# Performance work log

Measured on AMD Instinct MI355X. Metric: run time of the kernel, lower is better.

## Reference

```python
import jax, jax.numpy as jnp
import numpy as np

ALPHA = 0.5
EPS = 1e-6


def setup_inputs() -> dict:
    key = jax.random.key(0)
    k1, k2, k3 = jax.random.split(key, 3)
    B, N = 8192, 4096
    y_pred = jax.random.uniform(k1, (B, N), dtype=jnp.float32)
    y_true = jax.random.randint(k2, (B, N), 0, 2).astype(jnp.float32)
    depth_weights = jax.random.uniform(k3, (B, N), dtype=jnp.float32)
    return {"y_pred": y_pred, "y_true": y_true, "depth_weights": depth_weights}


def reference(y_pred, y_true, depth_weights):
    B, N = y_true.shape
    # --- weighted BCE ---
    bce = -(y_true * jnp.log(y_pred + EPS) + (1.0 - y_true) * jnp.log(1.0 - y_pred + EPS))
    wbce = jnp.mean(depth_weights * bce)

    # --- continuity-weighted loss: max run of correct predictions per row ---
    y_bin = (y_pred > 0.5).astype(y_true.dtype)
    correct = (y_bin == y_true)  # bool [B, N]
    idx = jnp.arange(N, dtype=jnp.int32)
    # position (1-based) of most recent incorrect element; 0 if none yet
    reset = jnp.where(correct, 0, idx + 1)  # [B, N]
    last_reset = jax.lax.cummax(reset, axis=1)  # [B, N]
    streak = (idx + 1)[None, :] - last_reset  # current run length at each position
    max_streak = jnp.max(streak, axis=1).astype(jnp.float32)  # [B]
    cwl = jnp.mean(1.0 - max_streak / N)

    return ALPHA * wbce + (1.0 - ALPHA) * cwl
```

## Files before the change

### kernel.cpp

```cpp
#include <hip/hip_runtime.h>

#define EPS 1e-6f
#define LN2F 0.69314718055994530942f

struct RunStats { int len, pre, suf, mx; };

__device__ inline RunStats rcombine(const RunStats& a, const RunStats& b) {
    RunStats r;
    r.len = a.len + b.len;
    r.pre = (a.pre == a.len) ? (a.len + b.pre) : a.pre;
    r.suf = (b.suf == b.len) ? (b.len + a.suf) : b.suf;
    r.mx  = max(max(a.mx, b.mx), a.suf + b.pre);
    return r;
}

__global__ __launch_bounds__(256) void row_kernel(
        const float* __restrict__ yp, const float* __restrict__ yt,
        const float* __restrict__ dw,
        float* __restrict__ row_wbce, int* __restrict__ row_streak) {
    const int row  = blockIdx.x;
    const int lane = threadIdx.x & 63;
    const int wave = threadIdx.x >> 6;
    const long base = (long)row * 4096 + wave * 1024 + lane * 4;

    const float4* pp = (const float4*)(yp + base);
    const float4* tp = (const float4*)(yt + base);
    const float4* wp = (const float4*)(dw + base);

    float4 P[4], T[4], W[4];
    #pragma unroll
    for (int q = 0; q < 4; ++q) {
        P[q] = pp[q * 64];
        T[q] = tp[q * 64];
        W[q] = wp[q * 64];
    }

    float sum = 0.0f;
    unsigned nibs = 0;
    #pragma unroll
    for (int q = 0; q < 4; ++q) {
        const float pv[4] = {P[q].x, P[q].y, P[q].z, P[q].w};
        const float tv[4] = {T[q].x, T[q].y, T[q].z, T[q].w};
        const float wv[4] = {W[q].x, W[q].y, W[q].z, W[q].w};
        #pragma unroll
        for (int c = 0; c < 4; ++c) {
            const bool tb = tv[c] != 0.0f;
            const float sel = tb ? pv[c] : 1.0f - pv[c];
            sum = fmaf(wv[c], __log2f(sel + EPS), sum);
            const bool correct = (pv[c] > 0.5f) == tb;
            nibs |= (unsigned)correct << (8 * q + c);
        }
    }

    __shared__ unsigned nibbuf[256];
    nibbuf[wave * 64 + lane] = nibs;
    __syncthreads();
    const uint4 d = *(const uint4*)&nibbuf[wave * 64 + 4 * (lane & 15)];
    const int qs = (lane >> 4) * 8;
    const unsigned mask = ((d.x >> qs) & 0xFu)
                        | (((d.y >> qs) & 0xFu) << 4)
                        | (((d.z >> qs) & 0xFu) << 8)
                        | (((d.w >> qs) & 0xFu) << 12);

    const int pre = __builtin_ctz(~mask);
    const int suf = __builtin_clz(~(mask << 16));
    int mx;
    {
        const unsigned p1 = mask;
        const unsigned p2 = p1 & (p1 << 1);
        const unsigned p4 = p2 & (p2 << 2);
        const unsigned p8 = p4 & (p4 << 4);
        unsigned z; int len;
        if (p8)      { z = p8; len = 8; }
        else if (p4) { z = p4; len = 4; }
        else if (p2) { z = p2; len = 2; }
        else         { z = p1; len = 1; }
        { const unsigned t = (z << 8) & p8; if (t) { z = t; len += 8; } }
        { const unsigned t = (z << 4) & p4; if (t) { z = t; len += 4; } }
        { const unsigned t = (z << 2) & p2; if (t) { z = t; len += 2; } }
        { const unsigned t = (z << 1) & p1; if (t) { z = t; len += 1; } }
        mx = mask ? len : 0;
    }

    #pragma unroll
    for (int off = 32; off; off >>= 1) sum += __shfl_down(sum, off);

    int packed = pre | (suf << 10) | (mx << 20);
    int alen = 16;
    #pragma unroll
    for (int off = 1; off < 32; off <<= 1) {
        const int o = __shfl_down(packed, off);
        const int apre = packed & 1023, asuf = (packed >> 10) & 1023, amx = packed >> 20;
        const int bpre = o & 1023,      bsuf = (o >> 10) & 1023,      bmx = o >> 20;
        const int npre = (apre == alen) ? (alen + bpre) : apre;
        const int nsuf = (bsuf == alen) ? (alen + asuf) : bsuf;
        const int nmx  = max(max(amx, bmx), asuf + bpre);
        packed = npre | (nsuf << 10) | (nmx << 20);
        alen <<= 1;
    }
    RunStats g;
    {
        const int o = __shfl_down(packed, 32);
        const int apre = packed & 1023, asuf = (packed >> 10) & 1023, amx = packed >> 20;
        const int bpre = o & 1023,      bsuf = (o >> 10) & 1023,      bmx = o >> 20;
        g.len = 1024;
        g.pre = (apre == 512) ? (512 + bpre) : apre;
        g.suf = (bsuf == 512) ? (512 + asuf) : bsuf;
        g.mx  = max(max(amx, bmx), asuf + bpre);
    }

    __shared__ RunStats sstat[4];
    __shared__ float ssum[4];
    if (lane == 0) { sstat[wave] = g; ssum[wave] = sum; }
    __syncthreads();
    if (threadIdx.x == 0) {
        RunStats r = rcombine(rcombine(sstat[0], sstat[1]), rcombine(sstat[2], sstat[3]));
        row_wbce[row]   = -LN2F * (ssum[0] + ssum[1] + ssum[2] + ssum[3]);
        row_streak[row] = r.mx;
    }
}

__global__ __launch_bounds__(1024) void finalize_kernel(
        const float* __restrict__ row_wbce, const int* __restrict__ row_streak,
        int rows, float* __restrict__ out) {
    double s = 0.0;
    long long st = 0;
    for (int i = threadIdx.x; i < rows; i += 1024) {
        s  += (double)row_wbce[i];
        st += (long long)row_streak[i];
    }
    __shared__ double sd[1024];
    __shared__ long long sl[1024];
    sd[threadIdx.x] = s; sl[threadIdx.x] = st;
    __syncthreads();
    for (int o = 512; o; o >>= 1) {
        if (threadIdx.x < o) {
            sd[threadIdx.x] += sd[threadIdx.x + o];
            sl[threadIdx.x] += sl[threadIdx.x + o];
        }
        __syncthreads();
    }
    if (threadIdx.x == 0) {
        const double total = (double)rows * 4096.0;
        const double wbce = sd[0] / total;
        const double cwl  = 1.0 - (double)sl[0] / total;
        out[0] = (float)(0.5 * wbce + 0.5 * cwl);
    }
}

extern "C" void kernel_launch(void* const* d_in, const int* in_sizes, int n_in,
                              void* d_out, int out_size, void* d_ws, size_t ws_size,
                              hipStream_t stream) {
    const float* yp = (const float*)d_in[0];
    const float* yt = (const float*)d_in[1];
    const float* dw = (const float*)d_in[2];
    float* out = (float*)d_out;

    const int rows = in_sizes[0] / 4096;
    float* row_wbce   = (float*)d_ws;
    int*   row_streak = (int*)((char*)d_ws + (size_t)rows * sizeof(float));

    row_kernel<<<rows, 256, 0, stream>>>(yp, yt, dw, row_wbce, row_streak);
    finalize_kernel<<<1, 1024, 0, stream>>>(row_wbce, row_streak, rows, out);
}
```

Measured before the change: 348.5 us.

## Process several rows per block with register double-buffered prefetch

Each block now handles four consecutive rows instead of one. While the current row is computed, the next row's inputs are loaded into a second register buffer. The first block-wide barrier is replaced by a wave-local LDS wait, which is enough because each wave only reads back its own mask words. Per-block partial sums are accumulated and written once, which shrinks the finalize input; the aim is more memory traffic in flight to hide load latency, at the cost of roughly doubled input registers and fewer blocks.

```diff
diff --git a/kernel.cpp b/kernel.cpp
--- a/kernel.cpp
+++ b/kernel.cpp
@@ -2,6 +2,7 @@
 
 #define EPS 1e-6f
 #define LN2F 0.69314718055994530942f
+#define ROWS_PER_BLOCK 4
 
 struct RunStats { int len, pre, suf, mx; };
 
@@ -14,120 +15,152 @@
     return r;
 }
 
-__global__ __launch_bounds__(256) void row_kernel(
+__global__ __launch_bounds__(256, 4) void row_kernel(
         const float* __restrict__ yp, const float* __restrict__ yt,
         const float* __restrict__ dw,
-        float* __restrict__ row_wbce, int* __restrict__ row_streak) {
-    const int row  = blockIdx.x;
+        float* __restrict__ blk_wbce, int* __restrict__ blk_streak) {
     const int lane = threadIdx.x & 63;
     const int wave = threadIdx.x >> 6;
-    const long base = (long)row * 4096 + wave * 1024 + lane * 4;
-
-    const float4* pp = (const float4*)(yp + base);
-    const float4* tp = (const float4*)(yt + base);
-    const float4* wp = (const float4*)(dw + base);
-
-    float4 P[4], T[4], W[4];
+    const int r0   = blockIdx.x * ROWS_PER_BLOCK;
+    const long tofs = (long)wave * 1024 + lane * 4;
+
+    __shared__ unsigned nibbuf[256];
+    __shared__ RunStats sstat[2][4];
+    __shared__ float    ssum[2][4];
+
+    float4 P[2][4], T[2][4], W[2][4];
+
+    {
+        const float4* pp = (const float4*)(yp + (long)r0 * 4096 + tofs);
+        const float4* tp = (const float4*)(yt + (long)r0 * 4096 + tofs);
+        const float4* wp = (const float4*)(dw + (long)r0 * 4096 + tofs);
+        #pragma unroll
+        for (int q = 0; q < 4; ++q) {
+            P[0][q] = pp[q * 64];
+            T[0][q] = tp[q * 64];
+            W[0][q] = wp[q * 64];
+        }
+    }
+
+    float acc_wbce   = 0.0f;
+    int   acc_streak = 0;
+
     #pragma unroll
-    for (int q = 0; q < 4; ++q) {
-        P[q] = pp[q * 64];
-        T[q] = tp[q * 64];
-        W[q] = wp[q * 64];
-    }
-
-    float sum = 0.0f;
-    unsigned nibs = 0;
-    #pragma unroll
-    for (int q = 0; q < 4; ++q) {
-        const float pv[4] = {P[q].x, P[q].y, P[q].z, P[q].w};
-        const float tv[4] = {T[q].x, T[q].y, T[q].z, T[q].w};
-        const float wv[4] = {W[q].x, W[q].y, W[q].z, W[q].w};
-        #pragma unroll
-        for (int c = 0; c < 4; ++c) {
-            const bool tb = tv[c] != 0.0f;
-            const float sel = tb ? pv[c] : 1.0f - pv[c];
-            sum = fmaf(wv[c], __log2f(sel + EPS), sum);
-            const bool correct = (pv[c] > 0.5f) == tb;
-            nibs |= (unsigned)correct << (8 * q + c);
-        }
-    }
-
-    __shared__ unsigned nibbuf[256];
-    nibbuf[wave * 64 + lane] = nibs;
-    __syncthreads();
-    const uint4 d = *(const uint4*)&nibbuf[wave * 64 + 4 * (lane & 15)];
-    const int qs = (lane >> 4) * 8;
-    const unsigned mask = ((d.x >> qs) & 0xFu)
-                        | (((d.y >> qs) & 0xFu) << 4)
-                        | (((d.z >> qs) & 0xFu) << 8)
-                        | (((d.w >> qs) & 0xFu) << 12);
-
-    const int pre = __builtin_ctz(~mask);
-    const int suf = __builtin_clz(~(mask << 16));
-    int mx;
-    {
-        const unsigned p1 = mask;
-        const unsigned p2 = p1 & (p1 << 1);
-        const unsigned p4 = p2 & (p2 << 2);
-        const unsigned p8 = p4 & (p4 << 4);
-        unsigned z; int len;
-        if (p8)      { z = p8; len = 8; }
-        else if (p4) { z = p4; len = 4; }
-        else if (p2) { z = p2; len = 2; }
-        else         { z = p1; len = 1; }
-        { const unsigned t = (z << 8) & p8; if (t) { z = t; len += 8; } }
-        { const unsigned t = (z << 4) & p4; if (t) { z = t; len += 4; } }
-        { const unsigned t = (z << 2) & p2; if (t) { z = t; len += 2; } }
-        { const unsigned t = (z << 1) & p1; if (t) { z = t; len += 1; } }
-        mx = mask ? len : 0;
-    }
-
-    #pragma unroll
-    for (int off = 32; off; off >>= 1) sum += __shfl_down(sum, off);
-
-    int packed = pre | (suf << 10) | (mx << 20);
-    int alen = 16;
-    #pragma unroll
-    for (int off = 1; off < 32; off <<= 1) {
-        const int o = __shfl_down(packed, off);
-        const int apre = packed & 1023, asuf = (packed >> 10) & 1023, amx = packed >> 20;
-        const int bpre = o & 1023,      bsuf = (o >> 10) & 1023,      bmx = o >> 20;
-        const int npre = (apre == alen) ? (alen + bpre) : apre;
-        const int nsuf = (bsuf == alen) ? (alen + asuf) : bsuf;
-        const int nmx  = max(max(amx, bmx), asuf + bpre);
-        packed = npre | (nsuf << 10) | (nmx << 20);
-        alen <<= 1;
-    }
-    RunStats g;
-    {
-        const int o = __shfl_down(packed, 32);
-        const int apre = packed & 1023, asuf = (packed >> 10) & 1023, amx = packed >> 20;
-        const int bpre = o & 1023,      bsuf = (o >> 10) & 1023,      bmx = o >> 20;
-        g.len = 1024;
-        g.pre = (apre == 512) ? (512 + bpre) : apre;
-        g.suf = (bsuf == 512) ? (512 + asuf) : bsuf;
-        g.mx  = max(max(amx, bmx), asuf + bpre);
-    }
-
-    __shared__ RunStats sstat[4];
-    __shared__ float ssum[4];
-    if (lane == 0) { sstat[wave] = g; ssum[wave] = sum; }
-    __syncthreads();
+    for (int r = 0; r < ROWS_PER_BLOCK; ++r) {
+        const int cur = r & 1;
+        const int nxt = cur ^ 1;
+
+        if (r + 1 < ROWS_PER_BLOCK) {
+            const float4* pp = (const float4*)(yp + (long)(r0 + r + 1) * 4096 + tofs);
+            const float4* tp = (const float4*)(yt + (long)(r0 + r + 1) * 4096 + tofs);
+            const float4* wp = (const float4*)(dw + (long)(r0 + r + 1) * 4096 + tofs);
+            #pragma unroll
+            for (int q = 0; q < 4; ++q) {
+                P[nxt][q] = pp[q * 64];
+                T[nxt][q] = tp[q * 64];
+                W[nxt][q] = wp[q * 64];
+            }
+        }
+        __builtin_amdgcn_sched_barrier(0);
+
+        float sum = 0.0f;
+        unsigned nibs = 0;
+        #pragma unroll
+        for (int q = 0; q < 4; ++q) {
+            const float pv[4] = {P[cur][q].x, P[cur][q].y, P[cur][q].z, P[cur][q].w};
+            const float tv[4] = {T[cur][q].x, T[cur][q].y, T[cur][q].z, T[cur][q].w};
+            const float wv[4] = {W[cur][q].x, W[cur][q].y, W[cur][q].z, W[cur][q].w};
+            #pragma unroll
+            for (int c = 0; c < 4; ++c) {
+                const bool tb = tv[c] != 0.0f;
+                const float sel = tb ? pv[c] : 1.0f - pv[c];
+                sum = fmaf(wv[c], __log2f(sel + EPS), sum);
+                const bool correct = (pv[c] > 0.5f) == tb;
+                nibs |= (unsigned)correct << (8 * q + c);
+            }
+        }
+
+        nibbuf[wave * 64 + lane] = nibs;
+        asm volatile("s_waitcnt lgkmcnt(0)" ::: "memory");
+        const uint4 d = *(const uint4*)&nibbuf[wave * 64 + 4 * (lane & 15)];
+        const int qs = (lane >> 4) * 8;
+        const unsigned mask = ((d.x >> qs) & 0xFu)
+                            | (((d.y >> qs) & 0xFu) << 4)
+                            | (((d.z >> qs) & 0xFu) << 8)
+                            | (((d.w >> qs) & 0xFu) << 12);
+
+        const int pre = __builtin_ctz(~mask);
+        const int suf = __builtin_clz(~(mask << 16));
+        int mx;
+        {
+            const unsigned p1 = mask;
+            const unsigned p2 = p1 & (p1 << 1);
+            const unsigned p4 = p2 & (p2 << 2);
+            const unsigned p8 = p4 & (p4 << 4);
+            unsigned z; int len;
+            if (p8)      { z = p8; len = 8; }
+            else if (p4) { z = p4; len = 4; }
+            else if (p2) { z = p2; len = 2; }
+            else         { z = p1; len = 1; }
+            { const unsigned t = (z << 8) & p8; if (t) { z = t; len += 8; } }
+            { const unsigned t = (z << 4) & p4; if (t) { z = t; len += 4; } }
+            { const unsigned t = (z << 2) & p2; if (t) { z = t; len += 2; } }
+            { const unsigned t = (z << 1) & p1; if (t) { z = t; len += 1; } }
+            mx = mask ? len : 0;
+        }
+
+        float wsum = sum;
+        #pragma unroll
+        for (int off = 32; off; off >>= 1) wsum += __shfl_down(wsum, off);
+
+        int packed = pre | (suf << 10) | (mx << 20);
+        int alen = 16;
+        #pragma unroll
+        for (int off = 1; off < 32; off <<= 1) {
+            const int o = __shfl_down(packed, off);
+            const int apre = packed & 1023, asuf = (packed >> 10) & 1023, amx = packed >> 20;
+            const int bpre = o & 1023,      bsuf = (o >> 10) & 1023,      bmx = o >> 20;
+            const int npre = (apre == alen) ? (alen + bpre) : apre;
+            const int nsuf = (bsuf == alen) ? (alen + asuf) : bsuf;
+            const int nmx  = max(max(amx, bmx), asuf + bpre);
+            packed = npre | (nsuf << 10) | (nmx << 20);
+            alen <<= 1;
+        }
+        RunStats g;
+        {
+            const int o = __shfl_down(packed, 32);
+            const int apre = packed & 1023, asuf = (packed >> 10) & 1023, amx = packed >> 20;
+            const int bpre = o & 1023,      bsuf = (o >> 10) & 1023,      bmx = o >> 20;
+            g.len = 1024;
+            g.pre = (apre == 512) ? (512 + bpre) : apre;
+            g.suf = (bsuf == 512) ? (512 + asuf) : bsuf;
+            g.mx  = max(max(amx, bmx), asuf + bpre);
+        }
+
+        if (lane == 0) { sstat[cur][wave] = g; ssum[cur][wave] = wsum; }
+        __syncthreads();
+        if (threadIdx.x == 0) {
+            RunStats rr = rcombine(rcombine(sstat[cur][0], sstat[cur][1]),
+                                   rcombine(sstat[cur][2], sstat[cur][3]));
+            acc_wbce   += ssum[cur][0] + ssum[cur][1] + ssum[cur][2] + ssum[cur][3];
+            acc_streak += rr.mx;
+        }
+    }
+
     if (threadIdx.x == 0) {
-        RunStats r = rcombine(rcombine(sstat[0], sstat[1]), rcombine(sstat[2], sstat[3]));
-        row_wbce[row]   = -LN2F * (ssum[0] + ssum[1] + ssum[2] + ssum[3]);
-        row_streak[row] = r.mx;
+        blk_wbce[blockIdx.x]   = -LN2F * acc_wbce;
+        blk_streak[blockIdx.x] = acc_streak;
     }
 }
 
 __global__ __launch_bounds__(1024) void finalize_kernel(
-        const float* __restrict__ row_wbce, const int* __restrict__ row_streak,
-        int rows, float* __restrict__ out) {
+        const float* __restrict__ blk_wbce, const int* __restrict__ blk_streak,
+        int nparts, long long total_elems, float* __restrict__ out) {
     double s = 0.0;
     long long st = 0;
-    for (int i = threadIdx.x; i < rows; i += 1024) {
-        s  += (double)row_wbce[i];
-        st += (long long)row_streak[i];
+    for (int i = threadIdx.x; i < nparts; i += 1024) {
+        s  += (double)blk_wbce[i];
+        st += (long long)blk_streak[i];
     }
     __shared__ double sd[1024];
     __shared__ long long sl[1024];
@@ -141,7 +174,7 @@
         __syncthreads();
     }
     if (threadIdx.x == 0) {
-        const double total = (double)rows * 4096.0;
+        const double total = (double)total_elems;
         const double wbce = sd[0] / total;
         const double cwl  = 1.0 - (double)sl[0] / total;
         out[0] = (float)(0.5 * wbce + 0.5 * cwl);
@@ -156,10 +189,13 @@
     const float* dw = (const float*)d_in[2];
     float* out = (float*)d_out;
 
-    const int rows = in_sizes[0] / 4096;
-    float* row_wbce   = (float*)d_ws;
-    int*   row_streak = (int*)((char*)d_ws + (size_t)rows * sizeof(float));
-
-    row_kernel<<<rows, 256, 0, stream>>>(yp, yt, dw, row_wbce, row_streak);
-    finalize_kernel<<<1, 1024, 0, stream>>>(row_wbce, row_streak, rows, out);
-}
+    const int rows    = in_sizes[0] / 4096;
+    const int nblocks = rows / ROWS_PER_BLOCK;
+
+    float* blk_wbce   = (float*)d_ws;
+    int*   blk_streak = (int*)((char*)d_ws + (size_t)nblocks * sizeof(float));
+
+    row_kernel<<<nblocks, 256, 0, stream>>>(yp, yt, dw, blk_wbce, blk_streak);
+    finalize_kernel<<<1, 1024, 0, stream>>>(blk_wbce, blk_streak, nblocks,
+                                            (long long)rows * 4096, out);
+}
```

Result: slower. 358.2 us (+2.8%).

## Split into persistent grid-stride mask/BCE pass and separate 64-bit run-length pass

Applied to the files above, without the earlier changes.

Replaces the one-block-per-row kernel with a persistent-style phase A kernel, launched as a fixed 2048-block grid. Each wave strides over 1024-element tiles, accumulates the weighted BCE and writes 16-bit correctness masks to the workspace. A phase B kernel then reads 256 masks per row and computes the longest correct run with 64-bit bit tricks and a 64-lane shuffle scan, and finalize reduces the per-wave partials. This is meant to remove the per-row block scheduling cost and the block-wide barrier, and to keep more loads in flight. In exchange it adds a small mask round-trip through memory and an extra kernel launch. It falls back to the old path if the workspace is too small.

```diff
diff --git a/kernel.cpp b/kernel.cpp
--- a/kernel.cpp
+++ b/kernel.cpp
@@ -3,8 +3,149 @@
 #define EPS 1e-6f
 #define LN2F 0.69314718055994530942f
 
+
+#define ONE(pc, tc, wc, bit) {                                   \
+    const bool  tb  = (tc) != 0.0f;   \
+    const float sel = tb ? (pc) : 1.0f - (pc);                   \
+    sum = fmaf((wc), __log2f(sel + EPS), sum);                   \
+    nibs |= (unsigned)(((pc) > 0.5f) == tb) << (bit); }
+
+#define CHUNK(P, T, W, q) {                  \
+    ONE(P.x, T.x, W.x, 8*(q)+0)              \
+    ONE(P.y, T.y, W.y, 8*(q)+1)              \
+    ONE(P.z, T.z, W.z, 8*(q)+2)              \
+    ONE(P.w, T.w, W.w, 8*(q)+3) }
+
+__global__ __launch_bounds__(256, 4) void phaseA_kernel(
+        const float* __restrict__ yp, const float* __restrict__ yt,
+        const float* __restrict__ dw,
+        unsigned short* __restrict__ masks,
+        float* __restrict__ wv_wbce,
+        long tiles_total) {
+    const int lane = threadIdx.x & 63;
+    const int wave = threadIdx.x >> 6;
+    const long wgid = (long)blockIdx.x * 4 + wave;
+    const long nwv  = (long)gridDim.x * 4;
+
+    __shared__ unsigned nibbuf[256];
+
+    float sum = 0.0f;
+
+    for (long t = wgid; t < tiles_total; t += nwv) {
+        const long base = t * 1024 + lane * 4;
+        const float4* pp = (const float4*)(yp + base);
+        const float4* tp = (const float4*)(yt + base);
+        const float4* wp = (const float4*)(dw + base);
+
+        const float4 p0 = pp[0],   p1 = pp[64],  p2 = pp[128], p3 = pp[192];
+        const float4 t0 = tp[0],   t1 = tp[64],  t2 = tp[128], t3 = tp[192];
+        const float4 w0 = wp[0],   w1 = wp[64],  w2 = wp[128], w3 = wp[192];
+
+        unsigned nibs = 0;
+        CHUNK(p0, t0, w0, 0)
+        CHUNK(p1, t1, w1, 1)
+        CHUNK(p2, t2, w2, 2)
+        CHUNK(p3, t3, w3, 3)
+
+        nibbuf[wave * 64 + lane] = nibs;
+        asm volatile("s_waitcnt lgkmcnt(0)" ::: "memory");
+        const uint4 d = *(const uint4*)&nibbuf[wave * 64 + 4 * (lane & 15)];
+        const int qs = (lane >> 4) * 8;
+        const unsigned mask = ((d.x >> qs) & 0xFu)
+                            | (((d.y >> qs) & 0xFu) << 4)
+                            | (((d.z >> qs) & 0xFu) << 8)
+                            | (((d.w >> qs) & 0xFu) << 12);
+        masks[t * 64 + (lane >> 4) * 16 + (lane & 15)] = (unsigned short)mask;
+    }
+
+    #pragma unroll
+    for (int off = 32; off; off >>= 1) sum += __shfl_down(sum, off);
+    if (lane == 0) wv_wbce[wgid] = sum;
+}
+
+__global__ __launch_bounds__(256, 4) void phaseB_kernel(
+        const unsigned short* __restrict__ masks,
+        int* __restrict__ wv_streak, long rows) {
+    const int lane = threadIdx.x & 63;
+    const int wave = threadIdx.x >> 6;
+    const long wgid = (long)blockIdx.x * 4 + wave;
+    const long nwv  = (long)gridDim.x * 4;
+
+    int acc = 0;
+    for (long r = wgid; r < rows; r += nwv) {
+        const unsigned long long m =
+            *(const unsigned long long*)(masks + r * 256 + lane * 4);
+        int pre, suf, mx;
+        if (~m == 0ULL) {
+            pre = suf = mx = 64;
+        } else {
+            pre = __builtin_ctzll(~m);
+            suf = __builtin_clzll(~m);
+            const unsigned long long pp1 = m;
+            const unsigned long long pp2 = pp1 & (pp1 << 1);
+            const unsigned long long pp4 = pp2 & (pp2 << 2);
+            const unsigned long long pp8 = pp4 & (pp4 << 4);
+            const unsigned long long pp16 = pp8 & (pp8 << 8);
+            const unsigned long long pp32 = pp16 & (pp16 << 16);
+            unsigned long long z; int len;
+            if (pp32)      { z = pp32; len = 32; }
+            else if (pp16) { z = pp16; len = 16; }
+            else if (pp8)  { z = pp8;  len = 8; }
+            else if (pp4)  { z = pp4;  len = 4; }
+            else if (pp2)  { z = pp2;  len = 2; }
+            else           { z = pp1;  len = 1; }
+            { const unsigned long long q = (z << 16) & pp16; if (q) { z = q; len += 16; } }
+            { const unsigned long long q = (z << 8)  & pp8;  if (q) { z = q; len += 8; } }
+            { const unsigned long long q = (z << 4)  & pp4;  if (q) { z = q; len += 4; } }
+            { const unsigned long long q = (z << 2)  & pp2;  if (q) { z = q; len += 2; } }
+            { const unsigned long long q = (z << 1)  & pp1;  if (q) { z = q; len += 1; } }
+            mx = m ? len : 0;
+        }
+
+        int alen = 64;
+        #pragma unroll
+        for (int off = 1; off < 64; off <<= 1) {
+            const int bpre = __shfl_down(pre, off);
+            const int bsuf = __shfl_down(suf, off);
+            const int bmx  = __shfl_down(mx,  off);
+            const int npre = (pre == alen) ? (alen + bpre) : pre;
+            const int nsuf = (bsuf == alen) ? (alen + suf) : bsuf;
+            mx  = max(max(mx, bmx), suf + bpre);
+            pre = npre; suf = nsuf; alen <<= 1;
+        }
+        if (lane == 0) acc += mx;
+    }
+    if (lane == 0) wv_streak[wgid] = acc;
+}
+
+__global__ __launch_bounds__(1024) void finalize_kernel(
+        const float* __restrict__ wv_wbce, int nA,
+        const int* __restrict__ wv_streak, int nB,
+        long long total_elems, float* __restrict__ out) {
+    double s = 0.0;
+    long long st = 0;
+    for (int i = threadIdx.x; i < nA; i += 1024) s  += (double)wv_wbce[i];
+    for (int i = threadIdx.x; i < nB; i += 1024) st += (long long)wv_streak[i];
+    __shared__ double sd[1024];
+    __shared__ long long sl[1024];
+    sd[threadIdx.x] = s; sl[threadIdx.x] = st;
+    __syncthreads();
+    for (int o = 512; o; o >>= 1) {
+        if (threadIdx.x < o) {
+            sd[threadIdx.x] += sd[threadIdx.x + o];
+            sl[threadIdx.x] += sl[threadIdx.x + o];
+        }
+        __syncthreads();
+    }
+    if (threadIdx.x == 0) {
+        const double total = (double)total_elems;
+        const double wbce = -LN2F * sd[0] / total;
+        const double cwl  = 1.0 - (double)sl[0] / total;
+        out[0] = (float)(0.5 * wbce + 0.5 * cwl);
+    }
+}
+
 struct RunStats { int len, pre, suf, mx; };
-
 __device__ inline RunStats rcombine(const RunStats& a, const RunStats& b) {
     RunStats r;
     r.len = a.len + b.len;
@@ -14,7 +155,7 @@
     return r;
 }
 
-__global__ __launch_bounds__(256) void row_kernel(
+__global__ __launch_bounds__(256) void fb_row_kernel(
         const float* __restrict__ yp, const float* __restrict__ yt,
         const float* __restrict__ dw,
         float* __restrict__ row_wbce, int* __restrict__ row_streak) {
@@ -22,93 +163,64 @@
     const int lane = threadIdx.x & 63;
     const int wave = threadIdx.x >> 6;
     const long base = (long)row * 4096 + wave * 1024 + lane * 4;
-
     const float4* pp = (const float4*)(yp + base);
     const float4* tp = (const float4*)(yt + base);
     const float4* wp = (const float4*)(dw + base);
 
-    float4 P[4], T[4], W[4];
-    #pragma unroll
-    for (int q = 0; q < 4; ++q) {
-        P[q] = pp[q * 64];
-        T[q] = tp[q * 64];
-        W[q] = wp[q * 64];
-    }
-
     float sum = 0.0f;
     unsigned nibs = 0;
     #pragma unroll
     for (int q = 0; q < 4; ++q) {
-        const float pv[4] = {P[q].x, P[q].y, P[q].z, P[q].w};
-        const float tv[4] = {T[q].x, T[q].y, T[q].z, T[q].w};
-        const float wv[4] = {W[q].x, W[q].y, W[q].z, W[q].w};
-        #pragma unroll
-        for (int c = 0; c < 4; ++c) {
-            const bool tb = tv[c] != 0.0f;
-            const float sel = tb ? pv[c] : 1.0f - pv[c];
-            sum = fmaf(wv[c], __log2f(sel + EPS), sum);
-            const bool correct = (pv[c] > 0.5f) == tb;
-            nibs |= (unsigned)correct << (8 * q + c);
-        }
-    }
-
+        const float4 P = pp[q * 64];
+        const float4 T = tp[q * 64];
+        const float4 W = wp[q * 64];
+        CHUNK(P, T, W, q)
+    }
     __shared__ unsigned nibbuf[256];
     nibbuf[wave * 64 + lane] = nibs;
     __syncthreads();
     const uint4 d = *(const uint4*)&nibbuf[wave * 64 + 4 * (lane & 15)];
     const int qs = (lane >> 4) * 8;
-    const unsigned mask = ((d.x >> qs) & 0xFu)
-                        | (((d.y >> qs) & 0xFu) << 4)
-                        | (((d.z >> qs) & 0xFu) << 8)
-                        | (((d.w >> qs) & 0xFu) << 12);
-
+    const unsigned mask = ((d.x >> qs) & 0xFu) | (((d.y >> qs) & 0xFu) << 4)
+                        | (((d.z >> qs) & 0xFu) << 8) | (((d.w >> qs) & 0xFu) << 12);
     const int pre = __builtin_ctz(~mask);
     const int suf = __builtin_clz(~(mask << 16));
     int mx;
     {
-        const unsigned p1 = mask;
-        const unsigned p2 = p1 & (p1 << 1);
-        const unsigned p4 = p2 & (p2 << 2);
-        const unsigned p8 = p4 & (p4 << 4);
+        const unsigned p1 = mask, p2 = p1 & (p1 << 1), p4 = p2 & (p2 << 2), p8 = p4 & (p4 << 4);
         unsigned z; int len;
-        if (p8)      { z = p8; len = 8; }
-        else if (p4) { z = p4; len = 4; }
-        else if (p2) { z = p2; len = 2; }
-        else         { z = p1; len = 1; }
-        { const unsigned t = (z << 8) & p8; if (t) { z = t; len += 8; } }
-        { const unsigned t = (z << 4) & p4; if (t) { z = t; len += 4; } }
-        { const unsigned t = (z << 2) & p2; if (t) { z = t; len += 2; } }
-        { const unsigned t = (z << 1) & p1; if (t) { z = t; len += 1; } }
+        if (p8) { z = p8; len = 8; } else if (p4) { z = p4; len = 4; }
+        else if (p2) { z = p2; len = 2; } else { z = p1; len = 1; }
+        { const unsigned q2 = (z << 8) & p8; if (q2) { z = q2; len += 8; } }
+        { const unsigned q2 = (z << 4) & p4; if (q2) { z = q2; len += 4; } }
+        { const unsigned q2 = (z << 2) & p2; if (q2) { z = q2; len += 2; } }
+        { const unsigned q2 = (z << 1) & p1; if (q2) { z = q2; len += 1; } }
         mx = mask ? len : 0;
     }
-
     #pragma unroll
     for (int off = 32; off; off >>= 1) sum += __shfl_down(sum, off);
-
     int packed = pre | (suf << 10) | (mx << 20);
     int alen = 16;
     #pragma unroll
     for (int off = 1; off < 32; off <<= 1) {
         const int o = __shfl_down(packed, off);
         const int apre = packed & 1023, asuf = (packed >> 10) & 1023, amx = packed >> 20;
-        const int bpre = o & 1023,      bsuf = (o >> 10) & 1023,      bmx = o >> 20;
-        const int npre = (apre == alen) ? (alen + bpre) : apre;
-        const int nsuf = (bsuf == alen) ? (alen + asuf) : bsuf;
-        const int nmx  = max(max(amx, bmx), asuf + bpre);
-        packed = npre | (nsuf << 10) | (nmx << 20);
+        const int bpre = o & 1023, bsuf = (o >> 10) & 1023, bmx = o >> 20;
+        packed = ((apre == alen) ? (alen + bpre) : apre)
+               | (((bsuf == alen) ? (alen + asuf) : bsuf) << 10)
+               | (max(max(amx, bmx), asuf + bpre) << 20);
         alen <<= 1;
     }
     RunStats g;
     {
         const int o = __shfl_down(packed, 32);
         const int apre = packed & 1023, asuf = (packed >> 10) & 1023, amx = packed >> 20;
-        const int bpre = o & 1023,      bsuf = (o >> 10) & 1023,      bmx = o >> 20;
+        const int bpre = o & 1023, bsuf = (o >> 10) & 1023, bmx = o >> 20;
         g.len = 1024;
         g.pre = (apre == 512) ? (512 + bpre) : apre;
         g.suf = (bsuf == 512) ? (512 + asuf) : bsuf;
         g.mx  = max(max(amx, bmx), asuf + bpre);
     }
-
     __shared__ RunStats sstat[4];
     __shared__ float ssum[4];
     if (lane == 0) { sstat[wave] = g; ssum[wave] = sum; }
@@ -120,31 +232,24 @@
     }
 }
 
-__global__ __launch_bounds__(1024) void finalize_kernel(
+__global__ __launch_bounds__(1024) void fb_finalize_kernel(
         const float* __restrict__ row_wbce, const int* __restrict__ row_streak,
         int rows, float* __restrict__ out) {
-    double s = 0.0;
-    long long st = 0;
+    double s = 0.0; long long st = 0;
     for (int i = threadIdx.x; i < rows; i += 1024) {
-        s  += (double)row_wbce[i];
-        st += (long long)row_streak[i];
+        s += (double)row_wbce[i]; st += (long long)row_streak[i];
     }
     __shared__ double sd[1024];
     __shared__ long long sl[1024];
     sd[threadIdx.x] = s; sl[threadIdx.x] = st;
     __syncthreads();
     for (int o = 512; o; o >>= 1) {
-        if (threadIdx.x < o) {
-            sd[threadIdx.x] += sd[threadIdx.x + o];
-            sl[threadIdx.x] += sl[threadIdx.x + o];
-        }
+        if (threadIdx.x < o) { sd[threadIdx.x] += sd[threadIdx.x + o]; sl[threadIdx.x] += sl[threadIdx.x + o]; }
         __syncthreads();
     }
     if (threadIdx.x == 0) {
         const double total = (double)rows * 4096.0;
-        const double wbce = sd[0] / total;
-        const double cwl  = 1.0 - (double)sl[0] / total;
-        out[0] = (float)(0.5 * wbce + 0.5 * cwl);
+        out[0] = (float)(0.5 * (sd[0] / total) + 0.5 * (1.0 - (double)sl[0] / total));
     }
 }
 
@@ -156,10 +261,27 @@
     const float* dw = (const float*)d_in[2];
     float* out = (float*)d_out;
 
-    const int rows = in_sizes[0] / 4096;
-    float* row_wbce   = (float*)d_ws;
-    int*   row_streak = (int*)((char*)d_ws + (size_t)rows * sizeof(float));
-
-    row_kernel<<<rows, 256, 0, stream>>>(yp, yt, dw, row_wbce, row_streak);
-    finalize_kernel<<<1, 1024, 0, stream>>>(row_wbce, row_streak, rows, out);
-}
+    const long rows = in_sizes[0] / 4096;
+    const long long total = (long long)rows * 4096;
+
+    const size_t mask_bytes = (size_t)rows * 512;
+    const size_t off_wbce   = mask_bytes;
+    const size_t off_streak = off_wbce + 8192 * sizeof(float);
+    const size_t need       = off_streak + 1024 * sizeof(int);
+
+    if (ws_size >= need) {
+        unsigned short* masks  = (unsigned short*)d_ws;
+        float* wv_wbce         = (float*)((char*)d_ws + off_wbce);
+        int*   wv_streak       = (int*)((char*)d_ws + off_streak);
+        const long tiles_total = total / 1024;
+
+        phaseA_kernel<<<2048, 256, 0, stream>>>(yp, yt, dw, masks, wv_wbce, tiles_total);
+        phaseB_kernel<<<256, 256, 0, stream>>>(masks, wv_streak, rows);
+        finalize_kernel<<<1, 1024, 0, stream>>>(wv_wbce, 8192, wv_streak, 1024, total, out);
+    } else {
+        float* row_wbce   = (float*)d_ws;
+        int*   row_streak = (int*)((char*)d_ws + (size_t)rows * sizeof(float));
+        fb_row_kernel<<<(int)rows, 256, 0, stream>>>(yp, yt, dw, row_wbce, row_streak);
+        fb_finalize_kernel<<<1, 1024, 0, stream>>>(row_wbce, row_streak, (int)rows, out);
+    }
+}
```

After: 360.7 us. 3.5% more time.
